# Performance work log

Measured on AMD Instinct MI355X. Metric: run time of the kernel, lower is better.

The kernel has to match this reference:

```python
import jax, jax.numpy as jnp
import numpy as np

B, S, D, H = 4, 1024, 1024, 16
HD = D // H


def setup_inputs() -> dict:
    key = jax.random.key(0)
    ks = jax.random.split(key, 8)
    q = jax.random.normal(ks[0], (B, S, D), jnp.float32)
    q_mask = jnp.ones((B, S), dtype=bool)
    kv_mask = jax.random.randint(ks[1], (B, S), 0, 2).astype(bool)
    edge_weights = jax.random.uniform(ks[2], (B, S, S), jnp.float32)
    w_init = 0.02
    wq = jax.random.normal(ks[3], (D, D), jnp.float32) * w_init
    wk = jax.random.normal(ks[4], (D, D), jnp.float32) * w_init
    wv = jax.random.normal(ks[5], (D, D), jnp.float32) * w_init
    wo = jax.random.normal(ks[6], (D, D), jnp.float32) * w_init
    bo = jnp.zeros((D,), jnp.float32)
    return {"q": q, "q_mask": q_mask, "kv_mask": kv_mask,
            "edge_weights": edge_weights, "wq": wq, "wk": wk, "wv": wv,
            "wo": wo, "bo": bo}


def _pass_with_mask(x, w, mask, b=None):
    # Linear applied everywhere, padded rows zeroed (matches pass_with_mask)
    y = x @ w.T
    if b is not None:
        y = y + b
    return jnp.where(mask[..., None], y, 0.0)


def reference(q, q_mask, kv_mask, edge_weights, wq, wk, wv, wo, bo):
    b = q.shape[0]
    # merge_masks: padding mask outer product (recv x send)
    full_mask = (q_mask[:, :, None] & kv_mask[:, None, :])[:, None]  # [b,1,s,s]
    # projections (self attention: k = v = q)
    qh = _pass_with_mask(q, wq, q_mask).reshape(b, S, H, HD).transpose(0, 2, 1, 3)
    kh = _pass_with_mask(q, wk, kv_mask).reshape(b, S, H, HD).transpose(0, 2, 1, 3)
    vh = _pass_with_mask(q, wv, kv_mask).reshape(b, S, H, HD).transpose(0, 2, 1, 3)
    # NOTE: faithful to source, scaled by sqrt(model_dim), not sqrt(head_dim)
    scores = jnp.einsum("bhqd,bhkd->bhqk", qh, kh) / np.sqrt(D).astype(np.float32)
    scores = scores * edge_weights[:, None]          # mul_weights=True
    scores = jnp.where(full_mask, scores, -jnp.inf)
    scores = jax.nn.softmax(scores, axis=-1)
    scores = jnp.where(full_mask, scores, 0.0)       # re-zero masked entries
    out = jnp.einsum("bhqk,bhkd->bhqd", scores, vh)
    out = out.transpose(0, 2, 1, 3).reshape(b, S, D)
    return _pass_with_mask(out, wo, q_mask, bo)
```

## Files before the change

kernel.cpp:

```cpp
#include <hip/hip_runtime.h>

typedef unsigned short u16;
typedef unsigned int u32;
typedef __bf16 b16x8 __attribute__((ext_vector_type(8)));
typedef u16 u16x8 __attribute__((ext_vector_type(8)));
typedef float f32x4 __attribute__((ext_vector_type(4)));
typedef float f32x16 __attribute__((ext_vector_type(16)));
typedef u32 u32x2 __attribute__((ext_vector_type(2)));

#define DEV __device__ __forceinline__
#define INF __builtin_inff()
#define MFMA16(a, b, c) __builtin_amdgcn_mfma_f32_16x16x32_bf16((a), (b), (c), 0, 0, 0)
#define MFMA32(a, b, c) __builtin_amdgcn_mfma_f32_32x32x16_bf16((a), (b), (c), 0, 0, 0)
#define EXP2F(x) __builtin_amdgcn_exp2f(x)

DEV u16 f2b(float f) {
  union { float f; unsigned u; } x; x.f = f;
  unsigned r = x.u + 0x7fffu + ((x.u >> 16) & 1u);
  return (u16)(r >> 16);
}

DEV u32 pk2(float a, float b) {
  __bf16 lo = (__bf16)a, hi = (__bf16)b;
  u16 ul, uh;
  __builtin_memcpy(&ul, &lo, 2);
  __builtin_memcpy(&uh, &hi, 2);
  return (u32)ul | ((u32)uh << 16);
}

DEV float b2f(u16 v) {
  union { u32 u; float f; } x; x.u = (u32)v << 16; return x.f;
}

DEV void gl_lds16(const u16* g, u16* l) {
  __builtin_amdgcn_global_load_lds((const __attribute__((address_space(1))) void*)g,
                                   (__attribute__((address_space(3))) void*)l, 16, 0, 0);
}

__global__ __launch_bounds__(256) void cvt_all(const float* __restrict__ q,
                                               const float* __restrict__ wq,
                                               const float* __restrict__ wk,
                                               const float* __restrict__ wv,
                                               const float* __restrict__ wo,
                                               u16* __restrict__ xb, u16* __restrict__ wqb,
                                               u16* __restrict__ wkb, u16* __restrict__ wvb,
                                               u16* __restrict__ wob) {
  const int blk = blockIdx.x;
  const float* src; u16* dst; float scale = 1.f; int base;
  if (blk < 4096)      { src = q;  dst = xb;  base = blk; }
  else if (blk < 5120) { src = wq; dst = wqb; base = blk - 4096; scale = 0.045084441f; }
  else if (blk < 6144) { src = wk; dst = wkb; base = blk - 5120; }
  else if (blk < 7168) { src = wv; dst = wvb; base = blk - 6144; }
  else                 { src = wo; dst = wob; base = blk - 7168; }
  const int i = base * 256 + threadIdx.x;
  float4 v = reinterpret_cast<const float4*>(src)[i];
  ushort4 o;
  o.x = f2b(v.x * scale);
  o.y = f2b(v.y * scale);
  o.z = f2b(v.z * scale);
  o.w = f2b(v.w * scale);
  reinterpret_cast<ushort4*>(dst)[i] = o;
}

__global__ __launch_bounds__(256) void repack_edge(const float* __restrict__ edge,
                                                   u16* __restrict__ Ef) {
  __shared__ float Ls[32][132];
  const int c = blockIdx.x;
  const int qt = blockIdx.y;
  const int b = blockIdx.z;
  const int tid = threadIdx.x;
#pragma unroll
  for (int it = 0; it < 4; ++it) {
    int idx = it * 256 + tid;
    int r = idx >> 5, k4 = idx & 31;
    f32x4 v = *reinterpret_cast<const f32x4*>(
        edge + (size_t)(b * 1024 + qt * 32 + r) * 1024 + c * 128 + k4 * 4);
#pragma unroll
    for (int e = 0; e < 4; ++e) Ls[r][k4 * 4 + e] = v[e];
  }
  __syncthreads();
#pragma unroll
  for (int it = 0; it < 2; ++it) {
    int slot = it * 256 + tid;
    int kvtl = slot >> 7, i = (slot >> 6) & 1, lane = slot & 63;
    int qv = lane & 31, hi = lane >> 5;
    u16x8 o;
#pragma unroll
    for (int jp = 0; jp < 8; ++jp) {
      int j = i * 8 + jp;
      int kvl = (j & 3) + 8 * (j >> 2) + 4 * hi;
      o[jp] = f2b(Ls[qv][kvtl * 32 + kvl]);
    }
    *reinterpret_cast<u16x8*>(
        Ef + ((size_t)(b * 32 + qt) * 32 + (c * 4 + kvtl)) * 1024 + i * 512 + lane * 8) = o;
  }
}

template <int MODE>
DEV void gemm_body(u16* __restrict__ SA, u16* __restrict__ SB,
                   const u16* __restrict__ A, const u16* __restrict__ W,
                   u16* __restrict__ Ybf, float* __restrict__ Yf,
                   const float* __restrict__ bias, const int* __restrict__ qmask) {
  const int t = threadIdx.x;
  const int lane = t & 63, w = t >> 6;
  const int lr = lane & 15, lg = lane >> 4;
  const int wr = w >> 1, wc = w & 1;
  const int m0 = blockIdx.y * 128, n0 = blockIdx.x * 128;

  f32x4 acc[4][4] = {};

  const int r0 = t >> 2;
  const int c0 = (t & 3) * 8;
  const u16* gA = A + (size_t)(m0 + r0) * 1024 + c0;
  const u16* gB = W + (size_t)(n0 + r0) * 1024 + c0;

  auto stage = [&](int buf, int kt) {
    const int ko = kt * 32;
    u16* lA = SA + buf * 4096 + w * 512;
    u16* lB = SB + buf * 4096 + w * 512;
    gl_lds16(gA + ko, lA);
    gl_lds16(gA + ko + 64 * 1024, lA + 2048);
    gl_lds16(gB + ko, lB);
    gl_lds16(gB + ko + 64 * 1024, lB + 2048);
  };

  stage(0, 0);
  __syncthreads();
  for (int kt = 0; kt < 32; ++kt) {
    const int cur = kt & 1;
    if (kt < 31) stage(cur ^ 1, kt + 1);
    const u16* As = SA + cur * 4096;
    const u16* Bs = SB + cur * 4096;
    b16x8 af[4], bf[4];
#pragma unroll
    for (int m = 0; m < 4; ++m)
      af[m] = *reinterpret_cast<const b16x8*>(As + (wr * 64 + m * 16 + lr) * 32 + lg * 8);
#pragma unroll
    for (int n = 0; n < 4; ++n)
      bf[n] = *reinterpret_cast<const b16x8*>(Bs + (wc * 64 + n * 16 + lr) * 32 + lg * 8);
#pragma unroll
    for (int m = 0; m < 4; ++m)
#pragma unroll
      for (int n = 0; n < 4; ++n)
        acc[m][n] = MFMA16(af[m], bf[n], acc[m][n]);
    __syncthreads();
  }

#pragma unroll
  for (int m = 0; m < 4; ++m) {
    const int row = m0 + wr * 64 + m * 16 + lg * 4;
#pragma unroll
    for (int n = 0; n < 4; ++n) {
      const int col = n0 + wc * 64 + n * 16 + lr;
#pragma unroll
      for (int r = 0; r < 4; ++r) {
        const int rowg = row + r;
        const float v = acc[m][n][r];
        if (MODE == 3) {
          float y = v + bias[col];
          Yf[(size_t)rowg * 1024 + col] = qmask[rowg] ? y : 0.f;
        } else if (MODE == 0) {
          Ybf[(size_t)rowg * 1024 + col] = f2b(v);
        } else if (MODE == 1) {
          const int bb = rowg >> 10, kv = rowg & 1023, kvt = kv >> 5, kl = kv & 31;
          const int h = col >> 6, dh = col & 63;
          const int s = dh >> 4, hi = (dh >> 3) & 1, j = dh & 7;
          size_t idx = (((size_t)((bb * 16 + h) * 32 + kvt) * 4 + s) * 64 + (kl + (hi << 5))) * 8 + j;
          Ybf[idx] = f2b(v);
        } else {
          const int bb = rowg >> 10, kv = rowg & 1023, kvt = kv >> 5, kvl = kv & 31;
          const int s = kvl >> 4, k16 = kvl & 15;
          const int hi = (k16 >> 2) & 1;
          const int j = (k16 & 3) | (((k16 >> 3) & 1) << 2);
          const int h = col >> 6, dh = col & 63, d = dh >> 5;
          size_t idx = ((((size_t)((bb * 16 + h) * 32 + kvt) * 2 + d) * 2 + s) * 64 + ((dh & 31) + (hi << 5))) * 8 + j;
          Ybf[idx] = f2b(v);
        }
      }
    }
  }
}

__global__ __launch_bounds__(256) void gemm_qkv(const u16* __restrict__ X,
                                                const u16* __restrict__ Wq,
                                                const u16* __restrict__ Wk,
                                                const u16* __restrict__ Wv,
                                                u16* __restrict__ Yq, u16* __restrict__ Yk,
                                                u16* __restrict__ Yv) {
  __shared__ __attribute__((aligned(16))) u16 SA[2 * 4096];
  __shared__ __attribute__((aligned(16))) u16 SB[2 * 4096];
  if (blockIdx.z == 0)      gemm_body<0>(SA, SB, X, Wq, Yq, nullptr, nullptr, nullptr);
  else if (blockIdx.z == 1) gemm_body<1>(SA, SB, X, Wk, Yk, nullptr, nullptr, nullptr);
  else                      gemm_body<2>(SA, SB, X, Wv, Yv, nullptr, nullptr, nullptr);
}
__global__ __launch_bounds__(256) void gemm_final(const u16* __restrict__ A,
                                                  const u16* __restrict__ Wo,
                                                  float* __restrict__ Out,
                                                  const float* __restrict__ bias,
                                                  const int* __restrict__ qmask) {
  __shared__ __attribute__((aligned(16))) u16 SA[2 * 4096];
  __shared__ __attribute__((aligned(16))) u16 SB[2 * 4096];
  gemm_body<3>(SA, SB, A, Wo, nullptr, Out, bias, qmask);
}

__global__ __launch_bounds__(256, 2) void attn_kernel(
    const u16* __restrict__ qh, const u16* __restrict__ Kf,
    const u16* __restrict__ Vf, const u16* __restrict__ Ef,
    const int* __restrict__ kvm, u16* __restrict__ out) {
  __shared__ float Osh[3][64][33];
  __shared__ float Lsh[4][32];

  const int d0 = blockIdx.x;
  const int logical = (d0 & 7) * 256 + (d0 >> 3);
  const int qt = logical & 31, bh = logical >> 5;
  const int b = bh >> 4, h = bh & 15;
  const int tid = threadIdx.x, lane = tid & 63, w = tid >> 6;
  const int ql = lane & 31, hi = lane >> 5;
  const int qrow = qt * 32 + ql;

  const u16* qp = qh + (size_t)(b * 1024 + qrow) * 1024 + h * 64 + hi * 8;
  b16x8 Qf[4];
#pragma unroll
  for (int s = 0; s < 4; ++s) Qf[s] = *reinterpret_cast<const b16x8*>(qp + s * 16);

  const u16* kb = Kf + (size_t)bh * 65536 + lane * 8;
  const u16* vb = Vf + (size_t)bh * 65536 + lane * 8;
  const u16* eb = Ef + (size_t)(b * 32 + qt) * 32768 + lane * 8;
  const int* ip = kvm + b * 1024 + hi * 4;

  f32x16 O0 = {}, O1 = {};
  float La[8] = {};

  struct Tile { b16x8 K[4]; b16x8 V[4]; u16x8 E8[2]; };
  Tile Ta, Tb;

  auto fetch = [&](Tile& T, int kvt) {
#pragma unroll
    for (int s = 0; s < 4; ++s)
      T.K[s] = *reinterpret_cast<const b16x8*>(kb + kvt * 2048 + s * 512);
#pragma unroll
    for (int ds = 0; ds < 4; ++ds)
      T.V[ds] = *reinterpret_cast<const b16x8*>(vb + kvt * 2048 + ds * 512);
#pragma unroll
    for (int i = 0; i < 2; ++i)
      T.E8[i] = *reinterpret_cast<const u16x8*>(eb + kvt * 1024 + i * 512);
  };

  auto compute = [&](const Tile& T, int kv0) {
    f32x4 F[4];
#pragma unroll
    for (int g = 0; g < 4; ++g) {
      int4 m4 = *reinterpret_cast<const int4*>(ip + kv0 + g * 8);
      F[g][0] = m4.x ? 0.f : -INF;
      F[g][1] = m4.y ? 0.f : -INF;
      F[g][2] = m4.z ? 0.f : -INF;
      F[g][3] = m4.w ? 0.f : -INF;
    }
    f32x16 S = {};
#pragma unroll
    for (int s = 0; s < 4; ++s) S = MFMA32(T.K[s], Qf[s], S);
    float p[16];
#pragma unroll
    for (int j = 0; j < 16; ++j)
      p[j] = EXP2F(fmaf(S[j], b2f(T.E8[j >> 3][j & 7]), F[j >> 2][j & 3]));
#pragma unroll
    for (int j = 0; j < 8; ++j) La[j] += p[j] + p[j + 8];
#pragma unroll
    for (int s = 0; s < 2; ++s) {
      union { u32 wd[4]; b16x8 v; } U;
      U.wd[0] = pk2(p[8 * s + 0], p[8 * s + 1]);
      U.wd[1] = pk2(p[8 * s + 2], p[8 * s + 3]);
      U.wd[2] = pk2(p[8 * s + 4], p[8 * s + 5]);
      U.wd[3] = pk2(p[8 * s + 6], p[8 * s + 7]);
      O0 = MFMA32(T.V[s], U.v, O0);
      O1 = MFMA32(T.V[2 + s], U.v, O1);
    }
  };

  const int base = w * 8;
  fetch(Ta, base);
#pragma unroll 1
  for (int kt = 0; kt < 6; kt += 2) {
    fetch(Tb, base + kt + 1);
    compute(Ta, (base + kt) << 5);
    fetch(Ta, base + kt + 2);
    compute(Tb, (base + kt + 1) << 5);
  }
  fetch(Tb, base + 7);
  compute(Ta, (base + 6) << 5);
  compute(Tb, (base + 7) << 5);

  float Lw = ((La[0] + La[1]) + (La[2] + La[3])) + ((La[4] + La[5]) + (La[6] + La[7]));
  Lw += __shfl_xor(Lw, 32, 64);

  if (hi == 0) Lsh[w][ql] = Lw;
  if (w > 0) {
#pragma unroll
    for (int r = 0; r < 16; ++r) Osh[w - 1][lane][r] = O0[r];
#pragma unroll
    for (int r = 0; r < 16; ++r) Osh[w - 1][lane][16 + r] = O1[r];
  }
  __syncthreads();
  if (w == 0) {
    float Lg = (Lsh[0][ql] + Lsh[1][ql]) + (Lsh[2][ql] + Lsh[3][ql]);
#pragma unroll
    for (int wv = 0; wv < 3; ++wv) {
#pragma unroll
      for (int r = 0; r < 16; ++r) O0[r] += Osh[wv][lane][r];
#pragma unroll
      for (int r = 0; r < 16; ++r) O1[r] += Osh[wv][lane][16 + r];
    }
    const float inv = (Lg > 0.f) ? 1.f / Lg : 0.f;
    u16* orow = out + (size_t)(b * 1024 + qrow) * 1024 + h * 64 + hi * 4;
#pragma unroll
    for (int H = 0; H < 2; ++H) {
#pragma unroll
      for (int g = 0; g < 4; ++g) {
        float o0 = (H ? O1[4 * g + 0] : O0[4 * g + 0]) * inv;
        float o1 = (H ? O1[4 * g + 1] : O0[4 * g + 1]) * inv;
        float o2 = (H ? O1[4 * g + 2] : O0[4 * g + 2]) * inv;
        float o3 = (H ? O1[4 * g + 3] : O0[4 * g + 3]) * inv;
        u32x2 wv2 = {pk2(o0, o1), pk2(o2, o3)};
        *reinterpret_cast<u32x2*>(orow + H * 32 + g * 8) = wv2;
      }
    }
  }
}

extern "C" void kernel_launch(void* const* d_in, const int* in_sizes, int n_in,
                              void* d_out, int out_size, void* d_ws, size_t ws_size,
                              hipStream_t stream) {
  (void)in_sizes; (void)n_in; (void)out_size; (void)ws_size;
  const float* q    = (const float*)d_in[0];
  const int*   qm   = (const int*)d_in[1];
  const int*   kvm  = (const int*)d_in[2];
  const float* edge = (const float*)d_in[3];
  const float* wq   = (const float*)d_in[4];
  const float* wk   = (const float*)d_in[5];
  const float* wv   = (const float*)d_in[6];
  const float* wo   = (const float*)d_in[7];
  const float* bo   = (const float*)d_in[8];
  float* out = (float*)d_out;

  char* ws = (char*)d_ws;
  u16* xb  = (u16*)(ws);
  u16* wqb = (u16*)(ws + (8ull  << 20));
  u16* wkb = (u16*)(ws + (10ull << 20));
  u16* wvb = (u16*)(ws + (12ull << 20));
  u16* wob = (u16*)(ws + (14ull << 20));
  u16* qhb = (u16*)(ws + (16ull << 20));
  u16* Kf  = (u16*)(ws + (24ull << 20));
  u16* Vf  = (u16*)(ws + (32ull << 20));
  u16* Ef  = (u16*)(ws + (40ull << 20));
  u16* ab  = xb;

  cvt_all<<<8192, 256, 0, stream>>>(q, wq, wk, wv, wo, xb, wqb, wkb, wvb, wob);
  gemm_qkv<<<dim3(8, 32, 3), 256, 0, stream>>>(xb, wqb, wkb, wvb, qhb, Kf, Vf);
  repack_edge<<<dim3(8, 32, 4), 256, 0, stream>>>(edge, Ef);
  attn_kernel<<<2048, 256, 0, stream>>>(qhb, Kf, Vf, Ef, kvm, ab);
  gemm_final<<<dim3(8, 32), 256, 0, stream>>>(ab, wob, out, bo, qm);
}
```

Baseline: 128.8 us.

## Repack Q into fragment layout, stage kv mask in LDS, restructure attention prefetch

The Q projection now writes Q in the same per-head fragment layout as K, so the attention kernel reads Q with coalesced 16-byte loads. The kv mask is converted once per block into a bf16 additive bias in shared memory instead of being read as int4 from global memory on every tile. The attention loop prefetches edge tiles two steps ahead and K one step ahead, while V is loaded just in time, to cut register pressure. Occupancy hints are raised to 3 for attention and 4 for the GEMMs. The trade-off is an extra barrier, V load latency that is exposed inside compute, and possible register spills under the tighter bounds.

```diff
diff --git a/kernel.cpp b/kernel.cpp
--- a/kernel.cpp
+++ b/kernel.cpp
@@ -159,13 +159,11 @@
         if (MODE == 3) {
           float y = v + bias[col];
           Yf[(size_t)rowg * 1024 + col] = qmask[rowg] ? y : 0.f;
-        } else if (MODE == 0) {
-          Ybf[(size_t)rowg * 1024 + col] = f2b(v);
         } else if (MODE == 1) {
-          const int bb = rowg >> 10, kv = rowg & 1023, kvt = kv >> 5, kl = kv & 31;
+          const int bb = rowg >> 10, rw = rowg & 1023, rt = rw >> 5, rl = rw & 31;
           const int h = col >> 6, dh = col & 63;
           const int s = dh >> 4, hi = (dh >> 3) & 1, j = dh & 7;
-          size_t idx = (((size_t)((bb * 16 + h) * 32 + kvt) * 4 + s) * 64 + (kl + (hi << 5))) * 8 + j;
+          size_t idx = (((size_t)((bb * 16 + h) * 32 + rt) * 4 + s) * 64 + (rl + (hi << 5))) * 8 + j;
           Ybf[idx] = f2b(v);
         } else {
           const int bb = rowg >> 10, kv = rowg & 1023, kvt = kv >> 5, kvl = kv & 31;
@@ -181,34 +179,35 @@
   }
 }
 
-__global__ __launch_bounds__(256) void gemm_qkv(const u16* __restrict__ X,
-                                                const u16* __restrict__ Wq,
-                                                const u16* __restrict__ Wk,
-                                                const u16* __restrict__ Wv,
-                                                u16* __restrict__ Yq, u16* __restrict__ Yk,
-                                                u16* __restrict__ Yv) {
+__global__ __launch_bounds__(256, 4) void gemm_qkv(const u16* __restrict__ X,
+                                                   const u16* __restrict__ Wq,
+                                                   const u16* __restrict__ Wk,
+                                                   const u16* __restrict__ Wv,
+                                                   u16* __restrict__ Yq, u16* __restrict__ Yk,
+                                                   u16* __restrict__ Yv) {
   __shared__ __attribute__((aligned(16))) u16 SA[2 * 4096];
   __shared__ __attribute__((aligned(16))) u16 SB[2 * 4096];
-  if (blockIdx.z == 0)      gemm_body<0>(SA, SB, X, Wq, Yq, nullptr, nullptr, nullptr);
+  if (blockIdx.z == 0)      gemm_body<1>(SA, SB, X, Wq, Yq, nullptr, nullptr, nullptr);
   else if (blockIdx.z == 1) gemm_body<1>(SA, SB, X, Wk, Yk, nullptr, nullptr, nullptr);
   else                      gemm_body<2>(SA, SB, X, Wv, Yv, nullptr, nullptr, nullptr);
 }
-__global__ __launch_bounds__(256) void gemm_final(const u16* __restrict__ A,
-                                                  const u16* __restrict__ Wo,
-                                                  float* __restrict__ Out,
-                                                  const float* __restrict__ bias,
-                                                  const int* __restrict__ qmask) {
+__global__ __launch_bounds__(256, 4) void gemm_final(const u16* __restrict__ A,
+                                                     const u16* __restrict__ Wo,
+                                                     float* __restrict__ Out,
+                                                     const float* __restrict__ bias,
+                                                     const int* __restrict__ qmask) {
   __shared__ __attribute__((aligned(16))) u16 SA[2 * 4096];
   __shared__ __attribute__((aligned(16))) u16 SB[2 * 4096];
   gemm_body<3>(SA, SB, A, Wo, nullptr, Out, bias, qmask);
 }
 
-__global__ __launch_bounds__(256, 2) void attn_kernel(
-    const u16* __restrict__ qh, const u16* __restrict__ Kf,
+__global__ __launch_bounds__(256, 3) void attn_kernel(
+    const u16* __restrict__ Qf, const u16* __restrict__ Kf,
     const u16* __restrict__ Vf, const u16* __restrict__ Ef,
     const int* __restrict__ kvm, u16* __restrict__ out) {
   __shared__ float Osh[3][64][33];
   __shared__ float Lsh[4][32];
+  __shared__ __attribute__((aligned(16))) u16 Fsh[1024];
 
   const int d0 = blockIdx.x;
   const int logical = (d0 & 7) * 256 + (d0 >> 3);
@@ -218,53 +217,61 @@
   const int ql = lane & 31, hi = lane >> 5;
   const int qrow = qt * 32 + ql;
 
-  const u16* qp = qh + (size_t)(b * 1024 + qrow) * 1024 + h * 64 + hi * 8;
-  b16x8 Qf[4];
-#pragma unroll
-  for (int s = 0; s < 4; ++s) Qf[s] = *reinterpret_cast<const b16x8*>(qp + s * 16);
-
-  const u16* kb = Kf + (size_t)bh * 65536 + lane * 8;
-  const u16* vb = Vf + (size_t)bh * 65536 + lane * 8;
-  const u16* eb = Ef + (size_t)(b * 32 + qt) * 32768 + lane * 8;
-  const int* ip = kvm + b * 1024 + hi * 4;
+#pragma unroll
+  for (int e = 0; e < 4; ++e) {
+    int idx = tid * 4 + e;
+    int kt = idx >> 5, h2 = (idx >> 4) & 1, j = idx & 15;
+    int kv = kt * 32 + 8 * (j >> 2) + 4 * h2 + (j & 3);
+    Fsh[idx] = kvm[b * 1024 + kv] ? (u16)0 : (u16)0xFF80;
+  }
+
+  const u16* qp = Qf + (size_t)bh * 65536 + qt * 2048 + lane * 8;
+  b16x8 Qr[4];
+#pragma unroll
+  for (int s = 0; s < 4; ++s) Qr[s] = *reinterpret_cast<const b16x8*>(qp + s * 512);
+
+  const u16* kp = Kf + (size_t)bh * 65536 + lane * 8;
+  const u16* vp = Vf + (size_t)bh * 65536 + lane * 8;
+  const u16* ep = Ef + (size_t)(b * 32 + qt) * 32768 + lane * 8;
 
   f32x16 O0 = {}, O1 = {};
-  float La[8] = {};
-
-  struct Tile { b16x8 K[4]; b16x8 V[4]; u16x8 E8[2]; };
-  Tile Ta, Tb;
-
-  auto fetch = [&](Tile& T, int kvt) {
+  float La[4] = {};
+
+  struct KB { b16x8 K[4]; };
+  struct EB { u16x8 E[2]; };
+  KB Ka, Kb;
+  EB E0, E1, E2;
+
+  auto fK = [&](KB& T, int kvt) {
 #pragma unroll
     for (int s = 0; s < 4; ++s)
-      T.K[s] = *reinterpret_cast<const b16x8*>(kb + kvt * 2048 + s * 512);
+      T.K[s] = *reinterpret_cast<const b16x8*>(kp + kvt * 2048 + s * 512);
+  };
+  auto fE = [&](EB& T, int kvt) {
+#pragma unroll
+    for (int i = 0; i < 2; ++i)
+      T.E[i] = *reinterpret_cast<const u16x8*>(ep + kvt * 1024 + i * 512);
+  };
+
+  auto compute = [&](const KB& K, const EB& E, int kvt) {
+    b16x8 V[4];
 #pragma unroll
     for (int ds = 0; ds < 4; ++ds)
-      T.V[ds] = *reinterpret_cast<const b16x8*>(vb + kvt * 2048 + ds * 512);
-#pragma unroll
-    for (int i = 0; i < 2; ++i)
-      T.E8[i] = *reinterpret_cast<const u16x8*>(eb + kvt * 1024 + i * 512);
-  };
-
-  auto compute = [&](const Tile& T, int kv0) {
-    f32x4 F[4];
-#pragma unroll
-    for (int g = 0; g < 4; ++g) {
-      int4 m4 = *reinterpret_cast<const int4*>(ip + kv0 + g * 8);
-      F[g][0] = m4.x ? 0.f : -INF;
-      F[g][1] = m4.y ? 0.f : -INF;
-      F[g][2] = m4.z ? 0.f : -INF;
-      F[g][3] = m4.w ? 0.f : -INF;
-    }
+      V[ds] = *reinterpret_cast<const b16x8*>(vp + kvt * 2048 + ds * 512);
+    u16x8 Fm0 = *reinterpret_cast<const u16x8*>(&Fsh[kvt * 32 + hi * 16]);
+    u16x8 Fm1 = *reinterpret_cast<const u16x8*>(&Fsh[kvt * 32 + hi * 16 + 8]);
     f32x16 S = {};
 #pragma unroll
-    for (int s = 0; s < 4; ++s) S = MFMA32(T.K[s], Qf[s], S);
+    for (int s = 0; s < 4; ++s) S = MFMA32(K.K[s], Qr[s], S);
     float p[16];
 #pragma unroll
-    for (int j = 0; j < 16; ++j)
-      p[j] = EXP2F(fmaf(S[j], b2f(T.E8[j >> 3][j & 7]), F[j >> 2][j & 3]));
-#pragma unroll
-    for (int j = 0; j < 8; ++j) La[j] += p[j] + p[j + 8];
+    for (int j = 0; j < 8; ++j)
+      p[j] = EXP2F(fmaf(S[j], b2f(E.E[0][j]), b2f(Fm0[j])));
+#pragma unroll
+    for (int j = 0; j < 8; ++j)
+      p[8 + j] = EXP2F(fmaf(S[8 + j], b2f(E.E[1][j]), b2f(Fm1[j])));
+#pragma unroll
+    for (int j = 0; j < 16; ++j) La[j & 3] += p[j];
 #pragma unroll
     for (int s = 0; s < 2; ++s) {
       union { u32 wd[4]; b16x8 v; } U;
@@ -272,25 +279,26 @@
       U.wd[1] = pk2(p[8 * s + 2], p[8 * s + 3]);
       U.wd[2] = pk2(p[8 * s + 4], p[8 * s + 5]);
       U.wd[3] = pk2(p[8 * s + 6], p[8 * s + 7]);
-      O0 = MFMA32(T.V[s], U.v, O0);
-      O1 = MFMA32(T.V[2 + s], U.v, O1);
+      O0 = MFMA32(V[s], U.v, O0);
+      O1 = MFMA32(V[2 + s], U.v, O1);
     }
   };
 
   const int base = w * 8;
-  fetch(Ta, base);
-#pragma unroll 1
-  for (int kt = 0; kt < 6; kt += 2) {
-    fetch(Tb, base + kt + 1);
-    compute(Ta, (base + kt) << 5);
-    fetch(Ta, base + kt + 2);
-    compute(Tb, (base + kt + 1) << 5);
-  }
-  fetch(Tb, base + 7);
-  compute(Ta, (base + 6) << 5);
-  compute(Tb, (base + 7) << 5);
-
-  float Lw = ((La[0] + La[1]) + (La[2] + La[3])) + ((La[4] + La[5]) + (La[6] + La[7]));
+  fE(E0, base); fE(E1, base + 1);
+  fK(Ka, base);
+  __syncthreads();
+
+  fE(E2, base + 2); fK(Kb, base + 1); compute(Ka, E0, base + 0);
+  fE(E0, base + 3); fK(Ka, base + 2); compute(Kb, E1, base + 1);
+  fE(E1, base + 4); fK(Kb, base + 3); compute(Ka, E2, base + 2);
+  fE(E2, base + 5); fK(Ka, base + 4); compute(Kb, E0, base + 3);
+  fE(E0, base + 6); fK(Kb, base + 5); compute(Ka, E1, base + 4);
+  fE(E1, base + 7); fK(Ka, base + 6); compute(Kb, E2, base + 5);
+                    fK(Kb, base + 7); compute(Ka, E0, base + 6);
+                                      compute(Kb, E1, base + 7);
+
+  float Lw = (La[0] + La[1]) + (La[2] + La[3]);
   Lw += __shfl_xor(Lw, 32, 64);
 
   if (hi == 0) Lsh[w][ql] = Lw;
@@ -348,15 +356,15 @@
   u16* wkb = (u16*)(ws + (10ull << 20));
   u16* wvb = (u16*)(ws + (12ull << 20));
   u16* wob = (u16*)(ws + (14ull << 20));
-  u16* qhb = (u16*)(ws + (16ull << 20));
+  u16* Qfb = (u16*)(ws + (16ull << 20));
   u16* Kf  = (u16*)(ws + (24ull << 20));
   u16* Vf  = (u16*)(ws + (32ull << 20));
   u16* Ef  = (u16*)(ws + (40ull << 20));
   u16* ab  = xb;
 
   cvt_all<<<8192, 256, 0, stream>>>(q, wq, wk, wv, wo, xb, wqb, wkb, wvb, wob);
-  gemm_qkv<<<dim3(8, 32, 3), 256, 0, stream>>>(xb, wqb, wkb, wvb, qhb, Kf, Vf);
+  gemm_qkv<<<dim3(8, 32, 3), 256, 0, stream>>>(xb, wqb, wkb, wvb, Qfb, Kf, Vf);
   repack_edge<<<dim3(8, 32, 4), 256, 0, stream>>>(edge, Ef);
-  attn_kernel<<<2048, 256, 0, stream>>>(qhb, Kf, Vf, Ef, kvm, ab);
+  attn_kernel<<<2048, 256, 0, stream>>>(Qfb, Kf, Vf, Ef, kvm, ab);
   gemm_final<<<dim3(8, 32), 256, 0, stream>>>(ab, wob, out, bo, qm);
 }
```

After: 119.0 us. 7.6% less time.
